# Kernel optimization log

Measured on AMD Instinct MI355X. Metric: run time of the kernel, lower is better.

The kernel has to match this reference:

```python
import jax, jax.numpy as jnp
import numpy as np
from jax.scipy.special import gammaln, xlogy

B, L, C = 8, 1024, 1536
H, KD, VD = 8, 64, 192
NF = 192              # num_features for relative positional basis
FS = NF // 6          # feat_size per basis family (each family emits 2*FS cols)
SCALE = KD ** -0.5


def _pos_basis(seq_len):
    """Enformer-style basis: [exp, central_mask, gamma], each concat'd with sign copy.
    Returns [2*seq_len-1, NF] float32 constants (no learnable params)."""
    positions = jnp.arange(-(seq_len - 1), seq_len, dtype=jnp.float32)
    seq_length = float(seq_len)
    ap = jnp.abs(positions)[:, None]                      # [2L-1, 1]
    # exponential decay features
    half_life = 2.0 ** jnp.linspace(3.0, np.log2(seq_length), FS)
    f_exp = jnp.exp(-jnp.log(2.0) / half_life * ap)       # [2L-1, FS]
    # central mask features
    cw = 2.0 ** jnp.arange(1, FS + 1, dtype=jnp.float32) - 1.0
    f_cm = (cw > ap).astype(jnp.float32)
    # gamma pdf features
    stddev = seq_length / (2.0 * FS)
    start_mean = seq_length / FS
    mean = jnp.linspace(start_mean, seq_length, FS)
    conc = (mean / stddev) ** 2
    rate = mean / stddev ** 2
    log_pdf = xlogy(conc - 1.0, ap) - rate * ap - gammaln(conc) + conc * jnp.log(rate)
    pdf = jnp.exp(log_pdf) + 1e-8
    f_g = pdf / jnp.max(pdf)
    sign = jnp.sign(positions)[:, None]
    feats = [f_exp, f_cm, f_g]
    return jnp.concatenate([jnp.concatenate([f, sign * f], axis=-1) for f in feats], axis=-1)


def _rel_shift(x):
    # x: [b, h, s, f]; Transformer-XL relative shift via pad+reshape.
    b, h, s, f = x.shape
    x = jnp.pad(x, ((0, 0), (0, 0), (0, 0), (1, 0)))
    x = x.reshape(b, h, f + 1, s)
    return x[:, :, 1:s + 1, :]


def setup_inputs() -> dict:
    key = jax.random.key(0)
    ks = jax.random.split(key, 12)
    s_in = C ** -0.5
    s_hv = (H * VD) ** -0.5
    s_nf = NF ** -0.5
    return {
        "x":  jax.random.normal(ks[0], (B, L, C), jnp.float32),
        "Wq": jax.random.normal(ks[1], (C, H * KD), jnp.float32) * s_in,
        "bq": jnp.zeros((H * KD,), jnp.float32),
        "Wk": jax.random.normal(ks[2], (C, H * KD), jnp.float32) * s_in,
        "bk": jnp.zeros((H * KD,), jnp.float32),
        "Wv": jax.random.normal(ks[3], (C, H * VD), jnp.float32) * s_in,
        "bv": jnp.zeros((H * VD,), jnp.float32),
        "Wo": jax.random.normal(ks[4], (H * VD, C), jnp.float32) * s_hv,
        "bo": jnp.zeros((C,), jnp.float32),
        "WR": jax.random.normal(ks[5], (NF, KD), jnp.float32) * s_nf,
        "u":  jax.random.normal(ks[6], (H, KD), jnp.float32) * 0.02,
        "v":  jax.random.normal(ks[7], (H, KD), jnp.float32) * 0.02,
    }


def reference(x, Wq, bq, Wk, bk, Wv, bv, Wo, bo, WR, u, v):
    b, s, c = x.shape
    Q = (x @ Wq + bq).reshape(b, s, H, KD).transpose(0, 2, 1, 3)   # [b,h,s,kd]
    K = (x @ Wk + bk).reshape(b, s, H, KD).transpose(0, 2, 1, 3)
    V = (x @ Wv + bv).reshape(b, s, H, VD).transpose(0, 2, 1, 3)
    R = _pos_basis(s) @ WR                                          # [2s-1, kd]
    term1 = jnp.einsum('bhqd,bhkd->bhqk', Q, K)                     # content-content
    term2 = _rel_shift(jnp.einsum('bhqd,rd->bhqr', Q, R))           # content-position
    term3 = jnp.einsum('hd,bhkd->bhk', u, K)[:, :, None, :]         # global content bias
    term4 = _rel_shift(jnp.einsum('hd,rd->hr', v, R)[None, :, None, :])  # [1,h,1,1]
    attn = jax.nn.softmax((term1 + term2 + term3 + term4) * SCALE, axis=-1)
    out = jnp.einsum('bhqk,bhkv->bhqv', attn, V)
    out = out.transpose(0, 2, 1, 3).reshape(b, s, H * VD)
    return out @ Wo + bo
```

## Files before the change

### kernel.cpp

```cpp
#include <hip/hip_runtime.h>
#include <cstdint>
#include <cstddef>
#include <cmath>

typedef float f32x4 __attribute__((ext_vector_type(4)));
typedef short bf16x8 __attribute__((ext_vector_type(8)));

#define DEVI __device__ __forceinline__

namespace {

constexpr int BB = 8, LL = 1024, CC = 1536;
constexpr int HH = 8, KDIM = 64, VDIM = 192;
constexpr int NFEAT = 192, FSZ = 32;
constexpr float SCL = 0.125f;
constexpr int MR = BB * LL;
constexpr int NQK = HH * KDIM;
constexpr int NVD = HH * VDIM;
constexpr int NQKV = 2 * NQK + NVD;

DEVI short f2bf(float f) {
  unsigned u = __float_as_uint(f);
  u = (u + 0x7FFFu + ((u >> 16) & 1u)) >> 16;
  return (short)u;
}

DEVI void gload_lds16(const void* g, void* l) {
  __builtin_amdgcn_global_load_lds(
      (const __attribute__((address_space(1))) void*)g,
      (__attribute__((address_space(3))) void*)l, 16, 0, 0);
}

__global__ void k_f32_to_bf16(const float* __restrict__ src, short* __restrict__ dst, int n) {
  int i0 = (blockIdx.x * blockDim.x + threadIdx.x) * 4;
  int stride = gridDim.x * blockDim.x * 4;
  for (int i = i0; i < n; i += stride) {
    float4 v = *reinterpret_cast<const float4*>(src + i);
    short4 o = { f2bf(v.x), f2bf(v.y), f2bf(v.z), f2bf(v.w) };
    *reinterpret_cast<short4*>(dst + i) = o;
  }
}

__global__ void k_transpose_all(const float* __restrict__ s0, short* __restrict__ d0,
                                const float* __restrict__ s1, short* __restrict__ d1,
                                const float* __restrict__ s2, short* __restrict__ d2,
                                const float* __restrict__ s3, short* __restrict__ d3) {
  __shared__ float tile[32][33];
  int idx = blockIdx.x;
  const float* src; short* dst; int R, Cd, gx, local;
  if (idx < 768)       { src = s0; dst = d0; R = CC;  Cd = NQK; gx = 16; local = idx; }
  else if (idx < 1536) { src = s1; dst = d1; R = CC;  Cd = NQK; gx = 16; local = idx - 768; }
  else if (idx < 3840) { src = s2; dst = d2; R = CC;  Cd = NVD; gx = 48; local = idx - 1536; }
  else                 { src = s3; dst = d3; R = NVD; Cd = CC;  gx = 48; local = idx - 3840; }
  int c0 = (local % gx) * 32, r0 = (local / gx) * 32;
  int tx = threadIdx.x, ty = threadIdx.y;
  #pragma unroll
  for (int i = 0; i < 4; i++)
    tile[ty + i * 8][tx] = src[(size_t)(r0 + ty + i * 8) * Cd + c0 + tx];
  __syncthreads();
  #pragma unroll
  for (int i = 0; i < 4; i++)
    dst[(size_t)(c0 + ty + i * 8) * R + r0 + tx] = f2bf(tile[tx][ty + i * 8]);
}

__global__ void k_build_r(const float* __restrict__ WR, float pmax,
                          short* __restrict__ rbuf) {
  __shared__ float feats[NFEAT];
  int jp = blockIdx.x;
  int tid = threadIdx.x;
  if (jp == 0) {
    if (tid < KDIM) rbuf[tid] = 0;
    return;
  }
  int j = jp - 1;
  int pos = j - (LL - 1);
  int api = pos < 0 ? -pos : pos;
  double ap = (double)api;
  float sgn = pos > 0 ? 1.0f : (pos < 0 ? -1.0f : 0.0f);
  if (tid < FSZ) {
    double xhl = 3.0 + 7.0 * (double)tid / 31.0;
    double hl = exp2(xhl);
    float fe = (float)exp2(-ap / hl);
    feats[tid] = fe; feats[FSZ + tid] = sgn * fe;
  } else if (tid < 2 * FSZ) {
    int i = tid - FSZ;
    double cw = exp2((double)(i + 1)) - 1.0;
    float fc = cw > ap ? 1.0f : 0.0f;
    feats[2 * FSZ + i] = fc; feats[3 * FSZ + i] = sgn * fc;
  } else if (tid < 3 * FSZ) {
    int i = tid - 2 * FSZ;
    double mean = 32.0 + 32.0 * (double)i;
    double conc = (mean * (1.0 / 16.0)) * (mean * (1.0 / 16.0));
    double rate = mean * (1.0 / 256.0);
    double lp = (conc - 1.0) * log(ap) - rate * ap - lgamma(conc) + conc * log(rate);
    double pdf = exp(lp) + 1e-8;
    float fg = (float)(pdf / (double)pmax);
    feats[4 * FSZ + i] = fg; feats[5 * FSZ + i] = sgn * fg;
  }
  __syncthreads();
  if (tid < KDIM) {
    float acc = 0.f;
    #pragma unroll 4
    for (int f = 0; f < NFEAT; f++) acc += feats[f] * WR[f * KDIM + tid];
    rbuf[jp * KDIM + tid] = f2bf(acc);
  }
}

template<int MODE>
__global__ __launch_bounds__(256, 3)
void k_gemm3(const short* __restrict__ A, const short* __restrict__ Bt,
             int Ndim, int Kdim,
             const float* __restrict__ c0, const float* __restrict__ c1,
             const float* __restrict__ c2, const float* __restrict__ c3,
             void* __restrict__ D0, void* __restrict__ D1,
             void* __restrict__ D2, void* __restrict__ D3) {
  __shared__ short sA[3][128][32];
  __shared__ short sB[3][128][32];

  int bid = blockIdx.x;
  int xcd = bid & 7;
  int s = bid >> 3;
  int mt = xcd * 8 + (s & 7);
  int nt = s >> 3;
  int m0 = mt * 128, n0 = nt * 128;
  int tid = threadIdx.x;
  int w = tid >> 6, l = tid & 63;
  int hi = l >> 4, lc = l & 15;
  int wr = (w >> 1) * 64, wc = (w & 1) * 64;

  int rowoff = l >> 2;
  int schunk = ((l & 3) ^ ((l >> 3) & 3)) * 8;
  const short* gA = A + (size_t)(m0 + rowoff) * Kdim + schunk;
  const short* gB = Bt + (size_t)(n0 + rowoff) * Kdim + schunk;

  f32x4 acc[4][4] = {};
  int T = Kdim >> 5;

  auto stage = [&](int d, int kt) {
    #pragma unroll
    for (int j = 0; j < 2; j++) {
      int rb = j * 64 + w * 16;
      gload_lds16(gA + (size_t)rb * Kdim + kt * 32, &sA[d][rb][0]);
      gload_lds16(gB + (size_t)rb * Kdim + kt * 32, &sB[d][rb][0]);
    }
  };

  stage(0, 0);
  stage(1, 1);
  asm volatile("s_waitcnt vmcnt(4)" ::: "memory");
  __builtin_amdgcn_s_barrier();
  __builtin_amdgcn_sched_barrier(0);

  int rswz = (lc >> 1) & 3;
  for (int t = 0; t < T; ++t) {
    int buf = t % 3;
    bool more = (t + 2) < T;
    if (more) stage((t + 2) % 3, t + 2);

    bf16x8 af[4], bfr[4];
    #pragma unroll
    for (int ni = 0; ni < 4; ni++)
      bfr[ni] = *(const bf16x8*)&sB[buf][wc + ni * 16 + lc][(hi ^ rswz) * 8];
    #pragma unroll
    for (int mi = 0; mi < 4; mi++)
      af[mi] = *(const bf16x8*)&sA[buf][wr + mi * 16 + lc][(hi ^ rswz) * 8];
    __builtin_amdgcn_s_setprio(1);
    #pragma unroll
    for (int mi = 0; mi < 4; mi++)
      #pragma unroll
      for (int ni = 0; ni < 4; ni++)
        acc[mi][ni] = __builtin_amdgcn_mfma_f32_16x16x32_bf16(af[mi], bfr[ni], acc[mi][ni], 0, 0, 0);
    __builtin_amdgcn_s_setprio(0);

    if (more) asm volatile("s_waitcnt vmcnt(4)" ::: "memory");
    else      asm volatile("s_waitcnt vmcnt(0)" ::: "memory");
    __builtin_amdgcn_s_barrier();
    __builtin_amdgcn_sched_barrier(0);
  }

  #pragma unroll
  for (int ni = 0; ni < 4; ni++) {
    int col = n0 + wc + ni * 16 + lc;
    if (MODE == 0) {
      if (col < NQK) {
        float bb = c0[col], uv = c3[col];
        #pragma unroll
        for (int mi = 0; mi < 4; mi++)
          #pragma unroll
          for (int rr = 0; rr < 4; rr++) {
            int row = m0 + wr + mi * 16 + hi * 4 + rr;
            float v = acc[mi][ni][rr] + bb;
            ((short*)D0)[(size_t)row * NQK + col] = f2bf(v * SCL);
            ((short*)D1)[(size_t)row * NQK + col] = f2bf((v + uv) * SCL);
          }
      } else if (col < 2 * NQK) {
        int c = col - NQK;
        float bb = c1[c];
        #pragma unroll
        for (int mi = 0; mi < 4; mi++)
          #pragma unroll
          for (int rr = 0; rr < 4; rr++) {
            int row = m0 + wr + mi * 16 + hi * 4 + rr;
            ((short*)D2)[(size_t)row * NQK + c] = f2bf(acc[mi][ni][rr] + bb);
          }
      } else {
        int c = col - 2 * NQK;
        int hh = c / VDIM, vv = c - hh * VDIM;
        float bb = c2[c];
        int bI = m0 >> 10;
        short* vt = (short*)D3 + ((size_t)(bI * 8 + hh) * VDIM + vv) * LL;
        int sbase = (m0 & (LL - 1)) + wr + hi * 4;
        #pragma unroll
        for (int mi = 0; mi < 4; mi++) {
          short4 o = { f2bf(acc[mi][ni][0] + bb), f2bf(acc[mi][ni][1] + bb),
                       f2bf(acc[mi][ni][2] + bb), f2bf(acc[mi][ni][3] + bb) };
          *(short4*)&vt[sbase + mi * 16] = o;
        }
      }
    } else {
      float bb = c0[col];
      #pragma unroll
      for (int mi = 0; mi < 4; mi++)
        #pragma unroll
        for (int rr = 0; rr < 4; rr++) {
          int row = m0 + wr + mi * 16 + hi * 4 + rr;
          ((float*)D0)[(size_t)row * Ndim + col] = acc[mi][ni][rr] + bb;
        }
    }
  }
}

__global__ __launch_bounds__(256, 2)
void k_attn(const short* __restrict__ Qp, const short* __restrict__ Qs,
            const short* __restrict__ Kb, const short* __restrict__ Vt,
            const short* __restrict__ Rb, short* __restrict__ AO) {
  __shared__ short sK[2][64][64];
  __shared__ short sV[2][192][64];
  __shared__ short sP[128][64];

  int bid = blockIdx.x;
  int swz = (bid & 7) * 64 + (bid >> 3);
  int qt = swz & 7, bh = swz >> 3;
  int b = bh >> 3, h = bh & 7;
  int q0 = qt * 128;
  int tid = threadIdx.x;
  int w = tid >> 6, l = tid & 63;
  int hi = l >> 4, lc = l & 15;

  int base = (w & 1) * 64;
  int par = w >> 1;
  int rbase = par ? 0 : 1024;

  bf16x8 aq1[2][2], aq2[2][2];
  #pragma unroll
  for (int mi = 0; mi < 2; mi++) {
    int qglob = q0 + base + par + 2 * (mi * 16 + lc);
    const short* qpg = Qp + (size_t)(b * LL + qglob) * NQK + h * KDIM;
    aq1[mi][0] = *(const bf16x8*)&qpg[hi * 8];
    aq1[mi][1] = *(const bf16x8*)&qpg[32 + hi * 8];
    int qsrow = q0 / 2 + base / 2 + par + mi * 16 + lc;
    const short* qsg = Qs + (size_t)(b * LL + qsrow) * NQK + h * KDIM;
    aq2[mi][0] = *(const bf16x8*)&qsg[hi * 8];
    aq2[mi][1] = *(const bf16x8*)&qsg[32 + hi * 8];
  }

  const short* kg = Kb + (size_t)(b * LL) * NQK + h * KDIM;
  const short* vg = Vt + (size_t)bh * VDIM * LL;
  const short* rg = Rb + (size_t)rbase * KDIM;

  int srow = l >> 3;
  int schunk = ((l & 7) ^ srow) * 8;

  float mrun[2][4], lrun[2][4];
  #pragma unroll
  for (int mi = 0; mi < 2; mi++)
    #pragma unroll
    for (int r = 0; r < 4; r++) { mrun[mi][r] = -INFINITY; lrun[mi][r] = 0.f; }
  f32x4 oacc[2][12] = {};

  #pragma unroll
  for (int j = 0; j < 2; j++) {
    int rb2 = (j * 4 + w) * 8;
    gload_lds16(kg + (size_t)(rb2 + srow) * NQK + schunk, &sK[0][rb2][0]);
  }
  #pragma unroll
  for (int j = 0; j < 6; j++) {
    int rb2 = (j * 4 + w) * 8;
    gload_lds16(vg + (size_t)(rb2 + srow) * LL + schunk, &sV[0][rb2][0]);
  }
  __syncthreads();

  int swzk = (lc & 7) << 3;

  for (int t = 0; t < 16; t++) {
    int k0 = t * 64;
    int bf = t & 1;

    bf16x8 br[2][4];
    #pragma unroll
    for (int kk = 0; kk < 2; kk++)
      #pragma unroll
      for (int ni = 0; ni < 4; ni++)
        br[kk][ni] = *(const bf16x8*)&rg[(size_t)(k0 + ni * 16 + lc) * KDIM + kk * 32 + hi * 8];

    if (t < 15) {
      int kn = k0 + 64;
      #pragma unroll
      for (int j = 0; j < 2; j++) {
        int rb2 = (j * 4 + w) * 8;
        gload_lds16(kg + (size_t)(kn + rb2 + srow) * NQK + schunk, &sK[bf ^ 1][rb2][0]);
      }
      #pragma unroll
      for (int j = 0; j < 6; j++) {
        int rb2 = (j * 4 + w) * 8;
        gload_lds16(vg + (size_t)(rb2 + srow) * LL + kn + schunk, &sV[bf ^ 1][rb2][0]);
      }
    }

    f32x4 s[2][4] = {};
    #pragma unroll
    for (int kk = 0; kk < 2; kk++) {
      #pragma unroll
      for (int ni = 0; ni < 4; ni++) {
        bf16x8 bk = *(const bf16x8*)&sK[bf][ni * 16 + lc][(kk * 32 + hi * 8) ^ swzk];
        #pragma unroll
        for (int mi = 0; mi < 2; mi++) {
          s[mi][ni] = __builtin_amdgcn_mfma_f32_16x16x32_bf16(aq1[mi][kk], bk, s[mi][ni], 0, 0, 0);
          s[mi][ni] = __builtin_amdgcn_mfma_f32_16x16x32_bf16(aq2[mi][kk], br[kk][ni], s[mi][ni], 0, 0, 0);
        }
      }
    }

    float lmx[2][4];
    float dmax = -INFINITY;
    #pragma unroll
    for (int mi = 0; mi < 2; mi++) {
      #pragma unroll
      for (int r = 0; r < 4; r++) {
        float m3 = fmaxf(fmaxf(s[mi][0][r], s[mi][1][r]), fmaxf(s[mi][2][r], s[mi][3][r]));
        lmx[mi][r] = m3;
        dmax = fmaxf(dmax, m3 - mrun[mi][r]);
      }
    }

    if (__any(dmax > 8.0f)) {
      #pragma unroll
      for (int mi = 0; mi < 2; mi++) {
        #pragma unroll
        for (int r = 0; r < 4; r++) {
          float m3 = lmx[mi][r];
          m3 = fmaxf(m3, __shfl_xor(m3, 1, 64));
          m3 = fmaxf(m3, __shfl_xor(m3, 2, 64));
          m3 = fmaxf(m3, __shfl_xor(m3, 4, 64));
          m3 = fmaxf(m3, __shfl_xor(m3, 8, 64));
          float mnew = fmaxf(mrun[mi][r], m3);
          float fc = __expf(mrun[mi][r] - mnew);
          mrun[mi][r] = mnew;
          lrun[mi][r] *= fc;
          #pragma unroll
          for (int ni = 0; ni < 12; ni++)
            oacc[mi][ni][r] *= fc;
        }
      }
    }

    #pragma unroll
    for (int mi = 0; mi < 2; mi++) {
      #pragma unroll
      for (int r = 0; r < 4; r++) {
        int prow = w * 32 + mi * 16 + 4 * hi + r;
        int pxor = ((4 * hi + r) & 7) << 3;
        float ps = 0.f;
        #pragma unroll
        for (int ni = 0; ni < 4; ni++) {
          float p = __expf(s[mi][ni][r] - mrun[mi][r]);
          ps += p;
          sP[prow][(ni * 16 + lc) ^ pxor] = f2bf(p);
        }
        lrun[mi][r] += ps;
      }
    }

    __builtin_amdgcn_s_setprio(1);
    #pragma unroll
    for (int kk = 0; kk < 2; kk++) {
      bf16x8 pa[2];
      #pragma unroll
      for (int mi = 0; mi < 2; mi++)
        pa[mi] = *(const bf16x8*)&sP[w * 32 + mi * 16 + lc][(kk * 32 + hi * 8) ^ swzk];
      #pragma unroll
      for (int ni = 0; ni < 12; ni++) {
        bf16x8 bv = *(const bf16x8*)&sV[bf][ni * 16 + lc][(kk * 32 + hi * 8) ^ swzk];
        #pragma unroll
        for (int mi = 0; mi < 2; mi++)
          oacc[mi][ni] = __builtin_amdgcn_mfma_f32_16x16x32_bf16(pa[mi], bv, oacc[mi][ni], 0, 0, 0);
      }
    }
    __builtin_amdgcn_s_setprio(0);

    __syncthreads();
  }

  #pragma unroll
  for (int mi = 0; mi < 2; mi++) {
    #pragma unroll
    for (int r = 0; r < 4; r++) {
      float L = lrun[mi][r];
      L += __shfl_xor(L, 1, 64);
      L += __shfl_xor(L, 2, 64);
      L += __shfl_xor(L, 4, 64);
      L += __shfl_xor(L, 8, 64);
      float iv = 1.0f / L;
      int qglob = q0 + base + par + 2 * (mi * 16 + 4 * hi + r);
      short* ao = AO + (size_t)(b * LL + qglob) * NVD + h * VDIM;
      #pragma unroll
      for (int ni = 0; ni < 12; ni++)
        ao[ni * 16 + lc] = f2bf(oacc[mi][ni][r] * iv);
    }
  }
}

}

extern "C" void kernel_launch(void* const* d_in, const int* in_sizes, int n_in,
                              void* d_out, int out_size, void* d_ws, size_t ws_size,
                              hipStream_t stream) {
  (void)in_sizes; (void)n_in; (void)out_size; (void)ws_size;
  const float* x  = (const float*)d_in[0];
  const float* Wq = (const float*)d_in[1];
  const float* bq = (const float*)d_in[2];
  const float* Wk = (const float*)d_in[3];
  const float* bk = (const float*)d_in[4];
  const float* Wv = (const float*)d_in[5];
  const float* bv = (const float*)d_in[6];
  const float* Wo = (const float*)d_in[7];
  const float* bo = (const float*)d_in[8];
  const float* WR = (const float*)d_in[9];
  const float* uu = (const float*)d_in[10];

  double pmaxd = 0.0;
  for (int i = 0; i < 32; i++) {
    double mean = 32.0 + 32.0 * (double)i;
    double conc = (mean / 16.0) * (mean / 16.0);
    double rate = mean / 256.0;
    double mode = (conc - 1.0) / rate;
    long m0i = (long)floor(mode);
    for (long dj = -2; dj <= 2; dj++) {
      long ap = m0i + dj;
      if (ap < 1) ap = 1;
      if (ap > 1023) ap = 1023;
      double lp = (conc - 1.0) * log((double)ap) - rate * (double)ap
                  - lgamma(conc) + conc * log(rate);
      double pdf = exp(lp) + 1e-8;
      if (pdf > pmaxd) pmaxd = pdf;
    }
  }
  float pmax = (float)pmaxd;

  char* ws = (char*)d_ws;
  size_t off = 0;
  auto alloc = [&](size_t bytes) -> void* {
    void* p = ws + off;
    off += (bytes + 255) & ~(size_t)255;
    return p;
  };
  short* RB      = (short*)alloc((size_t)2048 * 64 * 2);
  short* XB      = (short*)alloc((size_t)MR * CC * 2);
  short* WALL    = (short*)alloc((size_t)NQKV * CC * 2);
  short* WOT     = (short*)alloc((size_t)CC * NVD * 2);
  short* QP      = (short*)alloc((size_t)MR * NQK * 2);
  short* QS      = (short*)alloc((size_t)MR * NQK * 2);
  short* KB      = (short*)alloc((size_t)MR * NQK * 2);
  short* VT      = (short*)alloc((size_t)MR * NVD * 2);
  short* AO      = (short*)alloc((size_t)MR * NVD * 2);

  short* WQT = WALL;
  short* WKT = WALL + (size_t)NQK * CC;
  short* WVT = WALL + (size_t)(2 * NQK) * CC;

  k_f32_to_bf16<<<2048, 256, 0, stream>>>(x, XB, MR * CC);
  k_transpose_all<<<6144, dim3(32, 8), 0, stream>>>(Wq, WQT, Wk, WKT, Wv, WVT, Wo, WOT);
  k_build_r<<<2048, 256, 0, stream>>>(WR, pmax, RB);
  k_gemm3<0><<<dim3(MR / 128 * (NQKV / 128)), 256, 0, stream>>>(
      XB, WALL, NQKV, CC, bq, bk, bv, uu, QS, QP, KB, VT);
  k_attn<<<dim3(LL / 128 * BB * HH), 256, 0, stream>>>(QP, QS, KB, VT, RB, AO);
  k_gemm3<1><<<dim3(MR / 128 * (CC / 128)), 256, 0, stream>>>(
      AO, WOT, CC, NVD, bo, nullptr, nullptr, nullptr, d_out, nullptr, nullptr, nullptr);
}
```

Measured before the change: 244.2 us.

## Drop duplicate scaled-Q buffer and stage V transpose stores through LDS

The QKV GEMM epilogue now writes only one Q copy, (q+b+u)*scale, instead of two bf16 Q buffers. The attention kernel rebuilds the second copy on the fly by subtracting u*scale from the loaded values, which removes one full-size write and read of Q. The V-transpose epilogue now goes through LDS scratch so it can issue 16-byte coalesced stores instead of scattered 8-byte stores. Branching is also made uniform per tile. The cost is an extra bf16 rounding step on the reconstructed Q, plus LDS traffic and conversion work in the epilogue and in the attention prologue.

```diff
diff --git a/kernel.cpp b/kernel.cpp
--- a/kernel.cpp
+++ b/kernel.cpp
@@ -23,6 +23,10 @@
   unsigned u = __float_as_uint(f);
   u = (u + 0x7FFFu + ((u >> 16) & 1u)) >> 16;
   return (short)u;
+}
+
+DEVI float bf2f(short s) {
+  return __uint_as_float(((unsigned)(unsigned short)s) << 16);
 }
 
 DEVI void gload_lds16(const void* g, void* l) {
@@ -114,8 +118,7 @@
              const float* __restrict__ c2, const float* __restrict__ c3,
              void* __restrict__ D0, void* __restrict__ D1,
              void* __restrict__ D2, void* __restrict__ D3) {
-  __shared__ short sA[3][128][32];
-  __shared__ short sB[3][128][32];
+  __shared__ short sAB[2][3][128][32];
 
   int bid = blockIdx.x;
   int xcd = bid & 7;
@@ -140,8 +143,8 @@
     #pragma unroll
     for (int j = 0; j < 2; j++) {
       int rb = j * 64 + w * 16;
-      gload_lds16(gA + (size_t)rb * Kdim + kt * 32, &sA[d][rb][0]);
-      gload_lds16(gB + (size_t)rb * Kdim + kt * 32, &sB[d][rb][0]);
+      gload_lds16(gA + (size_t)rb * Kdim + kt * 32, &sAB[0][d][rb][0]);
+      gload_lds16(gB + (size_t)rb * Kdim + kt * 32, &sAB[1][d][rb][0]);
     }
   };
 
@@ -160,10 +163,10 @@
     bf16x8 af[4], bfr[4];
     #pragma unroll
     for (int ni = 0; ni < 4; ni++)
-      bfr[ni] = *(const bf16x8*)&sB[buf][wc + ni * 16 + lc][(hi ^ rswz) * 8];
+      bfr[ni] = *(const bf16x8*)&sAB[1][buf][wc + ni * 16 + lc][(hi ^ rswz) * 8];
     #pragma unroll
     for (int mi = 0; mi < 4; mi++)
-      af[mi] = *(const bf16x8*)&sA[buf][wr + mi * 16 + lc][(hi ^ rswz) * 8];
+      af[mi] = *(const bf16x8*)&sAB[0][buf][wr + mi * 16 + lc][(hi ^ rswz) * 8];
     __builtin_amdgcn_s_setprio(1);
     #pragma unroll
     for (int mi = 0; mi < 4; mi++)
@@ -178,23 +181,24 @@
     __builtin_amdgcn_sched_barrier(0);
   }
 
-  #pragma unroll
-  for (int ni = 0; ni < 4; ni++) {
-    int col = n0 + wc + ni * 16 + lc;
-    if (MODE == 0) {
-      if (col < NQK) {
-        float bb = c0[col], uv = c3[col];
+  if (MODE == 0) {
+    if (n0 < NQK) {
+      #pragma unroll
+      for (int ni = 0; ni < 4; ni++) {
+        int col = n0 + wc + ni * 16 + lc;
+        float bb = c0[col] + c3[col];
         #pragma unroll
         for (int mi = 0; mi < 4; mi++)
           #pragma unroll
           for (int rr = 0; rr < 4; rr++) {
             int row = m0 + wr + mi * 16 + hi * 4 + rr;
-            float v = acc[mi][ni][rr] + bb;
-            ((short*)D0)[(size_t)row * NQK + col] = f2bf(v * SCL);
-            ((short*)D1)[(size_t)row * NQK + col] = f2bf((v + uv) * SCL);
+            ((short*)D0)[(size_t)row * NQK + col] = f2bf((acc[mi][ni][rr] + bb) * SCL);
           }
-      } else if (col < 2 * NQK) {
-        int c = col - NQK;
+      }
+    } else if (n0 < 2 * NQK) {
+      #pragma unroll
+      for (int ni = 0; ni < 4; ni++) {
+        int c = n0 - NQK + wc + ni * 16 + lc;
         float bb = c1[c];
         #pragma unroll
         for (int mi = 0; mi < 4; mi++)
@@ -203,21 +207,40 @@
             int row = m0 + wr + mi * 16 + hi * 4 + rr;
             ((short*)D2)[(size_t)row * NQK + c] = f2bf(acc[mi][ni][rr] + bb);
           }
-      } else {
-        int c = col - 2 * NQK;
+      }
+    } else {
+      int c_base = n0 - 2 * NQK;
+      short* scr = &sAB[0][0][0][0] + w * (64 * 68);
+      float bbv[4];
+      #pragma unroll
+      for (int ni = 0; ni < 4; ni++) bbv[ni] = c2[c_base + wc + ni * 16 + lc];
+      #pragma unroll
+      for (int ni = 0; ni < 4; ni++)
+        #pragma unroll
+        for (int mi = 0; mi < 4; mi++)
+          #pragma unroll
+          for (int rr = 0; rr < 4; rr++)
+            scr[(mi * 16 + hi * 4 + rr) * 68 + ni * 16 + lc] =
+                f2bf(acc[mi][ni][rr] + bbv[ni]);
+      int bI = m0 >> 10;
+      int sgbase = (m0 & (LL - 1)) + wr;
+      #pragma unroll
+      for (int j = 0; j < 8; j++) {
+        int col_l = j * 8 + (l >> 3);
+        int s_l = (l & 7) * 8;
+        int c = c_base + wc + col_l;
         int hh = c / VDIM, vv = c - hh * VDIM;
-        float bb = c2[c];
-        int bI = m0 >> 10;
-        short* vt = (short*)D3 + ((size_t)(bI * 8 + hh) * VDIM + vv) * LL;
-        int sbase = (m0 & (LL - 1)) + wr + hi * 4;
-        #pragma unroll
-        for (int mi = 0; mi < 4; mi++) {
-          short4 o = { f2bf(acc[mi][ni][0] + bb), f2bf(acc[mi][ni][1] + bb),
-                       f2bf(acc[mi][ni][2] + bb), f2bf(acc[mi][ni][3] + bb) };
-          *(short4*)&vt[sbase + mi * 16] = o;
-        }
-      }
-    } else {
+        bf16x8 v8;
+        #pragma unroll
+        for (int e = 0; e < 8; e++) v8[e] = scr[(s_l + e) * 68 + col_l];
+        short* dst = (short*)D3 + ((size_t)(bI * 8 + hh) * VDIM + vv) * LL + sgbase + s_l;
+        *(bf16x8*)dst = v8;
+      }
+    }
+  } else {
+    #pragma unroll
+    for (int ni = 0; ni < 4; ni++) {
+      int col = n0 + wc + ni * 16 + lc;
       float bb = c0[col];
       #pragma unroll
       for (int mi = 0; mi < 4; mi++)
@@ -231,7 +254,7 @@
 }
 
 __global__ __launch_bounds__(256, 2)
-void k_attn(const short* __restrict__ Qp, const short* __restrict__ Qs,
+void k_attn(const short* __restrict__ Qp, const float* __restrict__ uu,
             const short* __restrict__ Kb, const short* __restrict__ Vt,
             const short* __restrict__ Rb, short* __restrict__ AO) {
   __shared__ short sK[2][64][64];
@@ -252,16 +275,29 @@
   int rbase = par ? 0 : 1024;
 
   bf16x8 aq1[2][2], aq2[2][2];
-  #pragma unroll
-  for (int mi = 0; mi < 2; mi++) {
-    int qglob = q0 + base + par + 2 * (mi * 16 + lc);
-    const short* qpg = Qp + (size_t)(b * LL + qglob) * NQK + h * KDIM;
-    aq1[mi][0] = *(const bf16x8*)&qpg[hi * 8];
-    aq1[mi][1] = *(const bf16x8*)&qpg[32 + hi * 8];
-    int qsrow = q0 / 2 + base / 2 + par + mi * 16 + lc;
-    const short* qsg = Qs + (size_t)(b * LL + qsrow) * NQK + h * KDIM;
-    aq2[mi][0] = *(const bf16x8*)&qsg[hi * 8];
-    aq2[mi][1] = *(const bf16x8*)&qsg[32 + hi * 8];
+  {
+    float u8[2][8];
+    #pragma unroll
+    for (int kk = 0; kk < 2; kk++)
+      #pragma unroll
+      for (int j = 0; j < 8; j++)
+        u8[kk][j] = uu[h * KDIM + kk * 32 + hi * 8 + j] * SCL;
+    #pragma unroll
+    for (int mi = 0; mi < 2; mi++) {
+      int qglob = q0 + base + par + 2 * (mi * 16 + lc);
+      const short* qpg = Qp + (size_t)(b * LL + qglob) * NQK + h * KDIM;
+      aq1[mi][0] = *(const bf16x8*)&qpg[hi * 8];
+      aq1[mi][1] = *(const bf16x8*)&qpg[32 + hi * 8];
+      int qsrow = q0 / 2 + base / 2 + par + mi * 16 + lc;
+      const short* qsg = Qp + (size_t)(b * LL + qsrow) * NQK + h * KDIM;
+      #pragma unroll
+      for (int kk = 0; kk < 2; kk++) {
+        bf16x8 t = *(const bf16x8*)&qsg[kk * 32 + hi * 8];
+        #pragma unroll
+        for (int j = 0; j < 8; j++)
+          aq2[mi][kk][j] = f2bf(bf2f(t[j]) - u8[kk][j]);
+      }
+    }
   }
 
   const short* kg = Kb + (size_t)(b * LL) * NQK + h * KDIM;
@@ -469,7 +505,6 @@
   short* WALL    = (short*)alloc((size_t)NQKV * CC * 2);
   short* WOT     = (short*)alloc((size_t)CC * NVD * 2);
   short* QP      = (short*)alloc((size_t)MR * NQK * 2);
-  short* QS      = (short*)alloc((size_t)MR * NQK * 2);
   short* KB      = (short*)alloc((size_t)MR * NQK * 2);
   short* VT      = (short*)alloc((size_t)MR * NVD * 2);
   short* AO      = (short*)alloc((size_t)MR * NVD * 2);
@@ -482,8 +517,8 @@
   k_transpose_all<<<6144, dim3(32, 8), 0, stream>>>(Wq, WQT, Wk, WKT, Wv, WVT, Wo, WOT);
   k_build_r<<<2048, 256, 0, stream>>>(WR, pmax, RB);
   k_gemm3<0><<<dim3(MR / 128 * (NQKV / 128)), 256, 0, stream>>>(
-      XB, WALL, NQKV, CC, bq, bk, bv, uu, QS, QP, KB, VT);
-  k_attn<<<dim3(LL / 128 * BB * HH), 256, 0, stream>>>(QP, QS, KB, VT, RB, AO);
+      XB, WALL, NQKV, CC, bq, bk, bv, uu, QP, nullptr, KB, VT);
+  k_attn<<<dim3(LL / 128 * BB * HH), 256, 0, stream>>>(QP, uu, KB, VT, RB, AO);
   k_gemm3<1><<<dim3(MR / 128 * (CC / 128)), 256, 0, stream>>>(
       AO, WOT, CC, NVD, bo, nullptr, nullptr, nullptr, d_out, nullptr, nullptr, nullptr);
 }
```

New measurement: 232.8 us, median of 2. -4.7%, faster.
